# Kernel optimization log

Hardware: AMD Instinct MI355X
Metric: run time of the kernel (lower is better)

## Reference

```python
import jax, jax.numpy as jnp
import numpy as np
from jax import lax

DIM = 1024
INNER = 2048  # dim * expand_factor
STATE = 64
B, T = 4, 2048
DECAY = 0.95
INPUT_FACTOR = 0.05
LN_EPS = 1e-5


def setup_inputs() -> dict:
    key = jax.random.key(0)
    ks = jax.random.split(key, 8)
    s = 0.02  # small weight scale
    return {
        "x": jax.random.normal(ks[0], (B, T, DIM), jnp.float32),
        "W_in": jax.random.normal(ks[1], (2 * INNER, DIM), jnp.float32) * s,
        "conv_w": jax.random.normal(ks[2], (INNER, 1, 4), jnp.float32) * s,
        "conv_b": jax.random.normal(ks[3], (INNER,), jnp.float32) * s,
        "W_B": jax.random.normal(ks[4], (STATE, INNER), jnp.float32) * s,
        "W_C": jax.random.normal(ks[5], (INNER, STATE), jnp.float32) * s,
        "D_param": jax.random.normal(ks[6], (INNER,), jnp.float32) * s,
        "W_out": jax.random.normal(ks[7], (DIM, INNER), jnp.float32) * s,
        "ln_gamma": jnp.ones((DIM,), jnp.float32),
        "ln_beta": jnp.zeros((DIM,), jnp.float32),
    }


def _layernorm(x, g, b):
    mu = jnp.mean(x, axis=-1, keepdims=True)
    var = jnp.mean(jnp.square(x - mu), axis=-1, keepdims=True)
    return (x - mu) * lax.rsqrt(var + LN_EPS) * g + b


def reference(x, W_in, conv_w, conv_b, W_B, W_C, D_param, W_out, ln_gamma, ln_beta):
    Bn, Tn, Dn = x.shape
    # in_proj -> split into input/gate halves
    x_proj = jnp.einsum("btd,ed->bte", x, W_in)  # [B,T,2*INNER]
    x_input, x_gate = jnp.split(x_proj, 2, axis=-1)
    # depthwise causal conv1d (torch pad=3 then slice [:T] == left-pad 3)
    xc = lax.conv_general_dilated(
        x_input.transpose(0, 2, 1),  # [B,C,T]
        conv_w,                       # [C,1,4]
        window_strides=(1,),
        padding=[(3, 0)],
        feature_group_count=INNER,
    ) + conv_b[None, :, None]
    u = jax.nn.silu(xc).transpose(0, 2, 1)  # [B,T,INNER]
    # linear recurrence: h_t = 0.95*h_{t-1} + 0.05*B_proj(u_t); h_0 = 0
    Bu = jnp.einsum("btc,sc->bts", u, W_B)  # [B,T,STATE]

    def step(h, bu_t):
        h = DECAY * h + INPUT_FACTOR * bu_t
        return h, h

    h0 = jnp.zeros((Bn, STATE), x.dtype)
    _, hs = lax.scan(step, h0, Bu.transpose(1, 0, 2))  # hs: [T,B,STATE]
    hs = hs.transpose(1, 0, 2)  # [B,T,STATE]
    y = jnp.einsum("bts,cs->btc", hs, W_C) + D_param * u  # [B,T,INNER]
    y = y * jax.nn.silu(x_gate)
    y = jnp.einsum("btc,dc->btd", y, W_out)  # [B,T,DIM]
    return _layernorm(y + x, ln_gamma, ln_beta)
```

## Files before the change

kernel.cpp:

```cpp
#include <hip/hip_runtime.h>
#include <hip/hip_bf16.h>

#define T_SEQ 2048
#define DIMD  1024
#define INNER 2048
#define STATE 64
#define BATCH 4
#define NCHUNK 64
#define CHUNK_L (T_SEQ / NCHUNK)
#define MROWS (BATCH * T_SEQ)
#define PSTRIDE ((long)MROWS * STATE)

typedef __hip_bfloat16 bf16;
typedef __attribute__((ext_vector_type(8))) short bf16x8v;
typedef __attribute__((ext_vector_type(4))) float f32x4v;
typedef __attribute__((ext_vector_type(4))) short short4v;

__device__ __forceinline__ float b2f(short s) {
    unsigned u = ((unsigned)(unsigned short)s) << 16;
    float f;
    __builtin_memcpy(&f, &u, 4);
    return f;
}
__device__ __forceinline__ short f2b(float f) {
    bf16 h = __float2bfloat16(f);
    short s;
    __builtin_memcpy(&s, &h, 2);
    return s;
}

__device__ __forceinline__ void gld_lds16(void* lds, const void* gsrc) {
    __builtin_amdgcn_global_load_lds(
        (const __attribute__((address_space(1))) unsigned*)gsrc,
        (__attribute__((address_space(3))) unsigned*)lds, 16, 0, 0);
}

template<int N> __device__ __forceinline__ void waitcnt_vm() {
    if constexpr (N == 16)      asm volatile("s_waitcnt vmcnt(16)" ::: "memory");
    else if constexpr (N == 8)  asm volatile("s_waitcnt vmcnt(8)" ::: "memory");
    else if constexpr (N == 6)  asm volatile("s_waitcnt vmcnt(6)" ::: "memory");
    else if constexpr (N == 4)  asm volatile("s_waitcnt vmcnt(4)" ::: "memory");
    else if constexpr (N == 2)  asm volatile("s_waitcnt vmcnt(2)" ::: "memory");
    else                        asm volatile("s_waitcnt vmcnt(0)" ::: "memory");
}
__device__ __forceinline__ void block_barrier() {
    asm volatile("" ::: "memory");
    __builtin_amdgcn_s_barrier();
    asm volatile("" ::: "memory");
}

template<int XSWZ>
__device__ __forceinline__ void swz_block(int& bx, int& by) {
    if constexpr (XSWZ == 1) {
        const int gx = gridDim.x;
        const int nwg = gx * gridDim.y;
        int id = by * gx + bx;
        const int cpx = nwg >> 3;
        id = (id & 7) * cpx + (id >> 3);
        bx = id % gx; by = id / gx;
    } else if constexpr (XSWZ == 2) {
        const int gx = gridDim.x;
        const int gy = gridDim.y;
        const int id = by * gx + bx;
        const int xcd = id & 7;
        const int c   = id >> 3;
        const int rowsX = gy >> 3;
        const int rw  = gx >> 2;
        const int r   = c >> 4;
        const int pos = c & 15;
        const int rbx = (r % rw) << 2;
        const int rby = (r / rw) << 2;
        bx = rbx + (pos & 3);
        by = xcd * rowsX + rby + (pos >> 2);
    }
}

template<int EPI, int XSWZ>
__global__ __launch_bounds__(512, 2)
void gemm_8ph(const short* __restrict__ A, const short* __restrict__ B,
              void* __restrict__ Cout, int M, int N, int K)
{
    __shared__ __align__(16) short As[2][2][128 * 64];
    __shared__ __align__(16) short Bs[2][2][128 * 64];

    int bx = blockIdx.x, by = blockIdx.y;
    swz_block<XSWZ>(bx, by);

    const int tid  = threadIdx.x;
    const int lane = tid & 63;
    const int wave = tid >> 6;
    const int wm2 = (wave >> 2) & 1;
    const int wn2 = wave & 3;
    const long bm = (long)by * 256;
    const long bn = (long)bx * 256;

    const int rsel = lane & 15;
    const int ssrc = (((tid & 7) ^ ((tid >> 3) & 7)) * 8);
    const int swz  = lane & 7;

    f32x4v acc[4][4][2];
#pragma unroll
    for (int q = 0; q < 4; q++)
#pragma unroll
        for (int m = 0; m < 4; m++)
#pragma unroll
            for (int n = 0; n < 2; n++)
                acc[q][m][n] = (f32x4v){0.f, 0.f, 0.f, 0.f};

    const int nt = K / 64;

    auto stage_half = [&](int tt, int h) {
        const int buf = tt & 1;
        const int half = h >> 1;
        const int k0 = tt * 64;
#pragma unroll
        for (int i = 0; i < 2; i++) {
            const int j = i * 512 + tid;
            if (h & 1)
                gld_lds16(&Bs[buf][half][j * 8],
                          &B[(bn + half * 128 + (j >> 3)) * (long)K + k0 + ssrc]);
            else
                gld_lds16(&As[buf][half][j * 8],
                          &A[(bm + half * 128 + (j >> 3)) * (long)K + k0 + ssrc]);
        }
    };

    stage_half(0, 0); stage_half(0, 1); stage_half(0, 2); stage_half(0, 3);

    for (int t = 0; t < nt; ++t) {
        const int buf = t & 1;
        const bool pf = (t + 1 < nt);
#pragma unroll
        for (int h = 0; h < 4; ++h) {
            if (pf) {
                if (h == 0) waitcnt_vm<4>();
                else if (h == 1) waitcnt_vm<4>();
                else if (h == 2) waitcnt_vm<4>();
            } else {
                if (h == 0) waitcnt_vm<4>();
                else if (h == 1) waitcnt_vm<2>();
                else if (h == 2) waitcnt_vm<0>();
            }
            block_barrier();

            const int QM[4] = {0, 1, 1, 0};
            const int QN[4] = {0, 0, 1, 1};
            const int qm = QM[h], qn = QN[h];
            bf16x8v af[4][2], bfv[2][2];
#pragma unroll
            for (int kkh = 0; kkh < 2; kkh++) {
                const int slog = kkh * 4 + (lane >> 4);
                const int soff = ((slog ^ swz) * 8);
#pragma unroll
                for (int m = 0; m < 4; m++) {
                    const int ar = wm2 * 64 + m * 16 + rsel;
                    af[m][kkh] = *(const bf16x8v*)&As[buf][qm][ar * 64 + soff];
                }
#pragma unroll
                for (int n = 0; n < 2; n++) {
                    const int br = wn2 * 32 + n * 16 + rsel;
                    bfv[n][kkh] = *(const bf16x8v*)&Bs[buf][qn][br * 64 + soff];
                }
            }
            if (pf) stage_half(t + 1, h);

            asm volatile("s_waitcnt lgkmcnt(0)" ::: "memory");
            __builtin_amdgcn_sched_barrier(0);
            __builtin_amdgcn_s_setprio(1);
#pragma unroll
            for (int kkh = 0; kkh < 2; kkh++)
#pragma unroll
                for (int m = 0; m < 4; m++)
#pragma unroll
                    for (int n = 0; n < 2; n++)
                        acc[h][m][n] = __builtin_amdgcn_mfma_f32_16x16x32_bf16(
                            af[m][kkh], bfv[n][kkh], acc[h][m][n], 0, 0, 0);
            __builtin_amdgcn_s_setprio(0);
        }
    }

#pragma unroll
    for (int q = 0; q < 4; q++) {
        const int QM[4] = {0, 1, 1, 0};
        const int QN[4] = {0, 0, 1, 1};
#pragma unroll
        for (int m = 0; m < 4; m++) {
#pragma unroll
            for (int n = 0; n < 2; n++) {
                const long col  = bn + QN[q] * 128 + wn2 * 32 + n * 16 + (lane & 15);
                const long row0 = bm + QM[q] * 128 + wm2 * 64 + m * 16 + (lane >> 4) * 4;
#pragma unroll
                for (int j = 0; j < 4; j++) {
                    const long idx = (row0 + j) * (long)N + col;
                    ((short*)Cout)[idx] = f2b(acc[q][m][n][j]);
                }
            }
        }
    }
}

template<int BM, int BN, int BK, int WR, int WC, int EPI, int SPLITK, int XSWZ>
__global__ __launch_bounds__(WR*WC*64, 2)
void gemm_ring(const short* __restrict__ A, const short* __restrict__ B,
               void* __restrict__ Cout, int M, int N, int K,
               const short* __restrict__ u_ptr, const short* __restrict__ gate_ptr,
               const float* __restrict__ Dp)
{
    constexpr int MFR = BM / (WR * 16);
    constexpr int NFR = BN / (WC * 16);
    constexpr int THREADS = WR * WC * 64;
    constexpr int UPR = BK / 8;
    constexpr int AISS = (BM * UPR) / THREADS;
    constexpr int BISS = (BN * UPR) / THREADS;
    constexpr int LPS  = AISS + BISS;
    __shared__ __align__(16) short As[2][BM * BK];
    __shared__ __align__(16) short Bs[2][BN * BK];

    int bx = blockIdx.x, by = blockIdx.y;
    swz_block<XSWZ>(bx, by);

    const int tid  = threadIdx.x;
    const int lane = tid & 63;
    const int wave = tid >> 6;
    const int wm = (wave / WC) * (MFR * 16);
    const int wn = (wave % WC) * (NFR * 16);
    const long bm = (long)by * BM;
    const long bn = (long)bx * BN;

    f32x4v acc[MFR][NFR];
#pragma unroll
    for (int m = 0; m < MFR; m++)
#pragma unroll
        for (int n = 0; n < NFR; n++)
            acc[m][n] = (f32x4v){0.f, 0.f, 0.f, 0.f};

    const int rsel = lane & 15;
    const int ssrc = (((tid & 7) ^ ((tid >> 3) & 7)) * 8);
    const int swz  = lane & 7;

    int kbeg = 0, kend = K;
    if constexpr (SPLITK > 1) {
        const int kch = K / SPLITK;
        kbeg = blockIdx.z * kch;
        kend = kbeg + kch;
    }
    const int nt = (kend - kbeg) / BK;

    auto stage = [&](int buf, int k0) {
#pragma unroll
        for (int i = 0; i < AISS; i++) {
            const int j = i * THREADS + tid;
            gld_lds16(&As[buf][j * 8],
                      &A[(bm + (j >> 3)) * (long)K + k0 + ssrc]);
        }
#pragma unroll
        for (int i = 0; i < BISS; i++) {
            const int j = i * THREADS + tid;
            gld_lds16(&Bs[buf][j * 8],
                      &B[(bn + (j >> 3)) * (long)K + k0 + ssrc]);
        }
    };
    auto compute = [&](int buf) {
#pragma unroll
        for (int kk = 0; kk < BK; kk += 32) {
            const int slog = (kk >> 3) + (lane >> 4);
            const int soff = ((slog ^ swz) * 8);
            bf16x8v af[MFR], bfv[NFR];
#pragma unroll
            for (int m = 0; m < MFR; m++)
                af[m] = *(const bf16x8v*)&As[buf][(wm + m * 16 + rsel) * BK + soff];
#pragma unroll
            for (int n = 0; n < NFR; n++)
                bfv[n] = *(const bf16x8v*)&Bs[buf][(wn + n * 16 + rsel) * BK + soff];
#pragma unroll
            for (int m = 0; m < MFR; m++)
#pragma unroll
                for (int n = 0; n < NFR; n++)
                    acc[m][n] = __builtin_amdgcn_mfma_f32_16x16x32_bf16(
                        af[m], bfv[n], acc[m][n], 0, 0, 0);
        }
    };

    stage(0, kbeg);
    for (int t = 0; t < nt; ++t) {
        const bool pf = (t + 1 < nt);
        if (pf) stage((t + 1) & 1, kbeg + (t + 1) * BK);
        if (pf) waitcnt_vm<LPS>();
        else    waitcnt_vm<0>();
        block_barrier();
        compute(t & 1);
        block_barrier();
    }

    float* fout = (float*)Cout;
    if constexpr (SPLITK > 1)
        fout += (long)blockIdx.z * (long)M * N;

#pragma unroll
    for (int m = 0; m < MFR; m++) {
#pragma unroll
        for (int n = 0; n < NFR; n++) {
            const long col  = bn + wn + n * 16 + (lane & 15);
            const long row0 = bm + wm + m * 16 + (lane >> 4) * 4;
#pragma unroll
            for (int j = 0; j < 4; j++) {
                const long row = row0 + j;
                const float v = acc[m][n][j];
                const long idx = row * (long)N + col;
                if constexpr (EPI == 0) {
                    ((short*)Cout)[idx] = f2b(v);
                } else if constexpr (EPI == 1) {
                    fout[idx] = v;
                } else {
                    ((short*)Cout)[idx] = f2b(v + b2f(u_ptr[idx]));
                }
            }
        }
    }
}

#define EBS 132
__global__ __launch_bounds__(256, 2)
void gemm3_fused(const short* __restrict__ hs, const short* __restrict__ Wc,
                 short* __restrict__ yg, const short* __restrict__ gate_ptr,
                 const float* __restrict__ Dp)
{
    __shared__ __align__(16) short As[128 * 64];
    __shared__ __align__(16) short Bs[128 * 64];
    __shared__ __align__(16) float eb[64 * EBS];

    const int tid  = threadIdx.x;
    const int lane = tid & 63;
    const int wave = tid >> 6;
    const int wm = (wave >> 1) * 64;
    const int wn = (wave & 1) * 64;
    const long bm = (long)blockIdx.y * 128;
    const long bn = (long)blockIdx.x * 128;

    const int rsel = lane & 15;
    const int ssrc = (((tid & 7) ^ ((tid >> 3) & 7)) * 8);
    const int swz  = lane & 7;

#pragma unroll
    for (int i = 0; i < 4; i++) {
        const int j = i * 256 + tid;
        gld_lds16(&As[j * 8], &hs[(bm + (j >> 3)) * (long)STATE + ssrc]);
    }
#pragma unroll
    for (int i = 0; i < 4; i++) {
        const int j = i * 256 + tid;
        gld_lds16(&Bs[j * 8], &Wc[(bn + (j >> 3)) * (long)STATE + ssrc]);
    }
    waitcnt_vm<0>();
    block_barrier();

    f32x4v acc[4][4];
#pragma unroll
    for (int m = 0; m < 4; m++)
#pragma unroll
        for (int n = 0; n < 4; n++)
            acc[m][n] = (f32x4v){0.f, 0.f, 0.f, 0.f};

#pragma unroll
    for (int kk = 0; kk < 64; kk += 32) {
        const int slog = (kk >> 3) + (lane >> 4);
        const int soff = ((slog ^ swz) * 8);
        bf16x8v af[4], bfv[4];
#pragma unroll
        for (int m = 0; m < 4; m++)
            af[m] = *(const bf16x8v*)&As[(wm + m * 16 + rsel) * 64 + soff];
#pragma unroll
        for (int n = 0; n < 4; n++)
            bfv[n] = *(const bf16x8v*)&Bs[(wn + n * 16 + rsel) * 64 + soff];
#pragma unroll
        for (int m = 0; m < 4; m++)
#pragma unroll
            for (int n = 0; n < 4; n++)
                acc[m][n] = __builtin_amdgcn_mfma_f32_16x16x32_bf16(
                    af[m], bfv[n], acc[m][n], 0, 0, 0);
    }

#pragma unroll
    for (int p = 0; p < 2; p++) {
        block_barrier();
        if ((wm >> 6) == p) {
#pragma unroll
            for (int m = 0; m < 4; m++) {
#pragma unroll
                for (int n = 0; n < 4; n++) {
                    const int cl = wn + n * 16 + (lane & 15);
#pragma unroll
                    for (int j = 0; j < 4; j++) {
                        const int rl = m * 16 + (lane >> 4) * 4 + j;
                        eb[rl * EBS + cl] = acc[m][n][j];
                    }
                }
            }
        }
        block_barrier();
#pragma unroll
        for (int k = 0; k < 4; k++) {
            const int unit = k * 256 + tid;
            const int rl = unit >> 4, cg = (unit & 15) * 8;
            const long grow = bm + p * 64 + rl;
            const long gcol = bn + cg;
            f32x4v y0 = *(const f32x4v*)&eb[rl * EBS + cg];
            f32x4v y1 = *(const f32x4v*)&eb[rl * EBS + cg + 4];
            bf16x8v uv = *(const bf16x8v*)&yg[grow * (long)INNER + gcol];
            bf16x8v gv = *(const bf16x8v*)&gate_ptr[grow * (long)(2 * INNER) + gcol];
            short o[8];
#pragma unroll
            for (int i = 0; i < 8; i++) {
                const float yy = (i < 4 ? y0[i] : y1[i - 4]);
                const float uu = b2f(uv[i]);
                const float gg = b2f(gv[i]);
                const float yv = yy + Dp[gcol + i] * uu;
                const float sg = gg / (1.f + __expf(-gg));
                o[i] = f2b(yv * sg);
            }
            *(bf16x8v*)&yg[grow * (long)INNER + gcol] = *(const bf16x8v*)o;
        }
    }
}

__global__ __launch_bounds__(256)
void conv_silu_kernel(const short* __restrict__ xproj, const float* __restrict__ cw,
                      const float* __restrict__ cb, short* __restrict__ u)
{
    const int bt = blockIdx.x;
    const int t  = bt & (T_SEQ - 1);
    const int c0 = threadIdx.x * 8;

    float wreg[4][8];
#pragma unroll
    for (int i = 0; i < 8; i++) {
        float4 wv = *(const float4*)&cw[(c0 + i) * 4];
        wreg[0][i] = wv.x; wreg[1][i] = wv.y; wreg[2][i] = wv.z; wreg[3][i] = wv.w;
    }
    float acc[8];
#pragma unroll
    for (int i = 0; i < 8; i++) acc[i] = cb[c0 + i];

#pragma unroll
    for (int k = 0; k < 4; k++) {
        if (t - 3 + k < 0) continue;
        bf16x8v v = *(const bf16x8v*)&xproj[(long)(bt - 3 + k) * (2 * INNER) + c0];
#pragma unroll
        for (int i = 0; i < 8; i++) acc[i] += b2f(v[i]) * wreg[k][i];
    }
    short o[8];
#pragma unroll
    for (int i = 0; i < 8; i++) {
        float s = acc[i] / (1.f + __expf(-acc[i]));
        o[i] = f2b(s);
    }
    *(bf16x8v*)&u[(long)bt * INNER + c0] = *(const bf16x8v*)o;
}

__global__ __launch_bounds__(64)
void scan_local_kernel(const float* __restrict__ Bu, float* __restrict__ locfin)
{
    const int b  = blockIdx.x / NCHUNK;
    const int ch = blockIdx.x % NCHUNK;
    const long base = ((long)b * T_SEQ + (long)ch * CHUNK_L) * STATE + threadIdx.x;
    float h = 0.f;
#pragma unroll
    for (int t = 0; t < CHUNK_L; t++) {
        const long o = base + (long)t * STATE;
        float bu = (Bu[o] + Bu[o + PSTRIDE]) + (Bu[o + 2 * PSTRIDE] + Bu[o + 3 * PSTRIDE]);
        h = 0.95f * h + 0.05f * bu;
    }
    locfin[(long)blockIdx.x * STATE + threadIdx.x] = h;
}

__global__ __launch_bounds__(256)
void carry_kernel(const float* __restrict__ locfin, float* __restrict__ carry,
                  float decayL)
{
    __shared__ float sm[BATCH * NCHUNK * STATE];
    for (int i = threadIdx.x; i < BATCH * NCHUNK * STATE; i += 256)
        sm[i] = locfin[i];
    __syncthreads();
    const int b = threadIdx.x >> 6, s = threadIdx.x & 63;
    float c = 0.f;
    for (int ch = 0; ch < NCHUNK; ch++) {
        const int idx = (b * NCHUNK + ch) * STATE + s;
        carry[idx] = c;
        c = decayL * c + sm[idx];
    }
}

__global__ __launch_bounds__(64)
void scan_apply_kernel(const float* __restrict__ Bu, const float* __restrict__ carry,
                       short* __restrict__ hs)
{
    const int b  = blockIdx.x / NCHUNK;
    const int ch = blockIdx.x % NCHUNK;
    const long base = ((long)b * T_SEQ + (long)ch * CHUNK_L) * STATE + threadIdx.x;
    float h = carry[(long)blockIdx.x * STATE + threadIdx.x];
#pragma unroll
    for (int t = 0; t < CHUNK_L; t++) {
        const long o = base + (long)t * STATE;
        float bu = (Bu[o] + Bu[o + PSTRIDE]) + (Bu[o + 2 * PSTRIDE] + Bu[o + 3 * PSTRIDE]);
        h = 0.95f * h + 0.05f * bu;
        hs[o] = f2b(h);
    }
}

__global__ __launch_bounds__(256)
void ln_kernel(const short* __restrict__ yx, const float* __restrict__ g,
               const float* __restrict__ b, float* __restrict__ out)
{
    const int row = blockIdx.x;
    const int c   = threadIdx.x * 4;
    const long off = (long)row * DIMD + c;
    const short4v yv = *(const short4v*)&yx[off];
    float s0 = b2f(yv[0]), s1 = b2f(yv[1]), s2 = b2f(yv[2]), s3 = b2f(yv[3]);
    float sum = s0 + s1 + s2 + s3;
    float sq  = s0 * s0 + s1 * s1 + s2 * s2 + s3 * s3;
#pragma unroll
    for (int o = 32; o > 0; o >>= 1) {
        sum += __shfl_down(sum, o);
        sq  += __shfl_down(sq, o);
    }
    __shared__ float rs[4], rq[4];
    const int wave = threadIdx.x >> 6, lane = threadIdx.x & 63;
    if (lane == 0) { rs[wave] = sum; rq[wave] = sq; }
    __syncthreads();
    float tsum = rs[0] + rs[1] + rs[2] + rs[3];
    float tsq  = rq[0] + rq[1] + rq[2] + rq[3];
    float mu  = tsum * (1.f / DIMD);
    float inv = rsqrtf(tsq * (1.f / DIMD) - mu * mu + 1e-5f);
    float4 gv = *(const float4*)&g[c];
    float4 bv = *(const float4*)&b[c];
    float4 ov;
    ov.x = (s0 - mu) * inv * gv.x + bv.x;
    ov.y = (s1 - mu) * inv * gv.y + bv.y;
    ov.z = (s2 - mu) * inv * gv.z + bv.z;
    ov.w = (s3 - mu) * inv * gv.w + bv.w;
    *(float4*)&out[off] = ov;
}

#define C4_X   2097152L
#define C4_W1  (C4_X + 1048576L)
#define C4_WB  (C4_W1 + 32768L)
#define C4_WC  (C4_WB + 32768L)
#define C4_TOT (C4_WC + 524288L)

__global__ __launch_bounds__(256)
void cvt5_kernel(const float* __restrict__ x, const float* __restrict__ w1,
                 const float* __restrict__ wB, const float* __restrict__ wC,
                 const float* __restrict__ wO, short* __restrict__ dst)
{
    const long i = (long)blockIdx.x * 256 + threadIdx.x;
    if (i >= C4_TOT) return;
    const float* s;
    long off;
    if      (i < C4_X)  { s = x;  off = i; }
    else if (i < C4_W1) { s = w1; off = i - C4_X; }
    else if (i < C4_WB) { s = wB; off = i - C4_W1; }
    else if (i < C4_WC) { s = wC; off = i - C4_WB; }
    else                { s = wO; off = i - C4_WC; }
    float4 v = *(const float4*)&s[off * 4];
    short4v o = { f2b(v.x), f2b(v.y), f2b(v.z), f2b(v.w) };
    *(short4v*)&dst[i * 4] = o;
}

extern "C" void kernel_launch(void* const* d_in, const int* in_sizes, int n_in,
                              void* d_out, int out_size, void* d_ws, size_t ws_size,
                              hipStream_t stream)
{
    const float* x     = (const float*)d_in[0];
    const float* W_in  = (const float*)d_in[1];
    const float* cw    = (const float*)d_in[2];
    const float* cb    = (const float*)d_in[3];
    const float* W_B   = (const float*)d_in[4];
    const float* W_C   = (const float*)d_in[5];
    const float* Dp    = (const float*)d_in[6];
    const float* W_out = (const float*)d_in[7];
    const float* ln_g  = (const float*)d_in[8];
    const float* ln_b  = (const float*)d_in[9];

    char* p = (char*)d_ws;
    short* xw    = (short*)(p);
    short* w1    = (short*)(p +  16777216);
    short* wB    = (short*)(p +  25165824);
    short* wC    = (short*)(p +  25427968);
    short* wO    = (short*)(p +  25690112);
    short* xproj = (short*)(p +  29884416);
    short* u     = (short*)(p +  96993280);
    short* hs    = (short*)(p + 132644864);
    short* yg    = u;
    short* yx    = xproj;
    float* BuP    = (float*)(p + 16777216);
    float* locfin = (float*)(p + 25165824);
    float* carry  = (float*)(p + 25231360);

    const int M = MROWS;

    cvt5_kernel<<<(int)((C4_TOT + 255) / 256), 256, 0, stream>>>(
        x, W_in, W_B, W_C, W_out, xw);

    gemm_8ph<0, 2><<<dim3(2 * INNER / 256, M / 256), 512, 0, stream>>>(
        xw, w1, xproj, M, 2 * INNER, DIMD);

    conv_silu_kernel<<<M, 256, 0, stream>>>(xproj, cw, cb, u);

    gemm_ring<64, 64, 64, 2, 2, 1, 4, 0><<<dim3(1, M / 64, 4), 256, 0, stream>>>(
        u, wB, BuP, M, STATE, INNER, nullptr, nullptr, nullptr);

    float decayL;
    {
        double dd = 1.0;
        for (int i = 0; i < CHUNK_L; i++) dd *= 0.95;
        decayL = (float)dd;
    }
    scan_local_kernel<<<BATCH * NCHUNK, STATE, 0, stream>>>(BuP, locfin);
    carry_kernel<<<1, 256, 0, stream>>>(locfin, carry, decayL);
    scan_apply_kernel<<<BATCH * NCHUNK, STATE, 0, stream>>>(BuP, carry, hs);

    gemm3_fused<<<dim3(INNER / 128, M / 128), 256, 0, stream>>>(
        hs, wC, yg, xproj + INNER, Dp);

    gemm_ring<128, 128, 64, 2, 2, 3, 1, 1><<<dim3(DIMD / 128, M / 128), 256, 0, stream>>>(
        yg, wO, yx, M, DIMD, INNER, xw, nullptr, nullptr);

    ln_kernel<<<M, 256, 0, stream>>>(yx, ln_g, ln_b, (float*)d_out);
}
```

Before: 242.8 us.

## Fuse causal conv+SiLU with B-projection GEMM, drop split-K partial sums

```diff
diff --git a/kernel.cpp b/kernel.cpp
--- a/kernel.cpp
+++ b/kernel.cpp
@@ -9,7 +9,6 @@
 #define NCHUNK 64
 #define CHUNK_L (T_SEQ / NCHUNK)
 #define MROWS (BATCH * T_SEQ)
-#define PSTRIDE ((long)MROWS * STATE)
 
 typedef __hip_bfloat16 bf16;
 typedef __attribute__((ext_vector_type(8))) short bf16x8v;
@@ -36,9 +35,7 @@
 }
 
 template<int N> __device__ __forceinline__ void waitcnt_vm() {
-    if constexpr (N == 16)      asm volatile("s_waitcnt vmcnt(16)" ::: "memory");
-    else if constexpr (N == 8)  asm volatile("s_waitcnt vmcnt(8)" ::: "memory");
-    else if constexpr (N == 6)  asm volatile("s_waitcnt vmcnt(6)" ::: "memory");
+    if constexpr (N == 8)       asm volatile("s_waitcnt vmcnt(8)" ::: "memory");
     else if constexpr (N == 4)  asm volatile("s_waitcnt vmcnt(4)" ::: "memory");
     else if constexpr (N == 2)  asm volatile("s_waitcnt vmcnt(2)" ::: "memory");
     else                        asm volatile("s_waitcnt vmcnt(0)" ::: "memory");
@@ -133,9 +130,7 @@
 #pragma unroll
         for (int h = 0; h < 4; ++h) {
             if (pf) {
-                if (h == 0) waitcnt_vm<4>();
-                else if (h == 1) waitcnt_vm<4>();
-                else if (h == 2) waitcnt_vm<4>();
+                if (h < 3) waitcnt_vm<4>();
             } else {
                 if (h == 0) waitcnt_vm<4>();
                 else if (h == 1) waitcnt_vm<2>();
@@ -199,12 +194,11 @@
     }
 }
 
-template<int BM, int BN, int BK, int WR, int WC, int EPI, int SPLITK, int XSWZ>
+template<int BM, int BN, int BK, int WR, int WC, int EPI, int XSWZ>
 __global__ __launch_bounds__(WR*WC*64, 2)
 void gemm_ring(const short* __restrict__ A, const short* __restrict__ B,
                void* __restrict__ Cout, int M, int N, int K,
-               const short* __restrict__ u_ptr, const short* __restrict__ gate_ptr,
-               const float* __restrict__ Dp)
+               const short* __restrict__ u_ptr)
 {
     constexpr int MFR = BM / (WR * 16);
     constexpr int NFR = BN / (WC * 16);
@@ -238,13 +232,7 @@
     const int ssrc = (((tid & 7) ^ ((tid >> 3) & 7)) * 8);
     const int swz  = lane & 7;
 
-    int kbeg = 0, kend = K;
-    if constexpr (SPLITK > 1) {
-        const int kch = K / SPLITK;
-        kbeg = blockIdx.z * kch;
-        kend = kbeg + kch;
-    }
-    const int nt = (kend - kbeg) / BK;
+    const int nt = K / BK;
 
     auto stage = [&](int buf, int k0) {
 #pragma unroll
@@ -281,20 +269,16 @@
         }
     };
 
-    stage(0, kbeg);
+    stage(0, 0);
     for (int t = 0; t < nt; ++t) {
         const bool pf = (t + 1 < nt);
-        if (pf) stage((t + 1) & 1, kbeg + (t + 1) * BK);
+        if (pf) stage((t + 1) & 1, (t + 1) * BK);
         if (pf) waitcnt_vm<LPS>();
         else    waitcnt_vm<0>();
         block_barrier();
         compute(t & 1);
         block_barrier();
     }
-
-    float* fout = (float*)Cout;
-    if constexpr (SPLITK > 1)
-        fout += (long)blockIdx.z * (long)M * N;
 
 #pragma unroll
     for (int m = 0; m < MFR; m++) {
@@ -309,12 +293,103 @@
                 const long idx = row * (long)N + col;
                 if constexpr (EPI == 0) {
                     ((short*)Cout)[idx] = f2b(v);
-                } else if constexpr (EPI == 1) {
-                    fout[idx] = v;
                 } else {
                     ((short*)Cout)[idx] = f2b(v + b2f(u_ptr[idx]));
                 }
             }
+        }
+    }
+}
+
+#define RB 32
+#define CK 256
+__global__ __launch_bounds__(256, 2)
+void conv_bu_kernel(const short* __restrict__ xproj, const float* __restrict__ cw,
+                    const float* __restrict__ cb, const short* __restrict__ wB,
+                    short* __restrict__ u, float* __restrict__ Bu)
+{
+    __shared__ __align__(16) short Us[RB * CK];
+    __shared__ __align__(16) short Ws[STATE * CK];
+
+    const int tid  = threadIdx.x;
+    const int lane = tid & 63;
+    const int wave = tid >> 6;
+    const int wm = (wave >> 1) * 16;
+    const int wn = (wave & 1) * 32;
+    const long r0 = (long)blockIdx.x * RB;
+    const int rsel = lane & 15;
+
+    f32x4v acc[2];
+    acc[0] = (f32x4v){0.f, 0.f, 0.f, 0.f};
+    acc[1] = (f32x4v){0.f, 0.f, 0.f, 0.f};
+
+    for (int ch = 0; ch < INNER / CK; ++ch) {
+        const int k0 = ch * CK;
+#pragma unroll
+        for (int i = 0; i < 8; i++) {
+            const int j = i * 256 + tid;
+            const int row = j >> 5, sp = j & 31;
+            const int sl = sp ^ (row & 7);
+            gld_lds16(&Ws[j * 8], &wB[(long)row * INNER + k0 + sl * 8]);
+        }
+#pragma unroll
+        for (int k = 0; k < 4; k++) {
+            const int unit = k * 256 + tid;
+            const int r = unit >> 5, cg = unit & 31;
+            const long grow = r0 + r;
+            const int t = (int)(grow & (T_SEQ - 1));
+            const int c = k0 + cg * 8;
+            float a[8];
+            {
+                float4 b0 = *(const float4*)&cb[c];
+                float4 b1 = *(const float4*)&cb[c + 4];
+                a[0]=b0.x; a[1]=b0.y; a[2]=b0.z; a[3]=b0.w;
+                a[4]=b1.x; a[5]=b1.y; a[6]=b1.z; a[7]=b1.w;
+            }
+#pragma unroll
+            for (int tap = 0; tap < 4; tap++) {
+                if (t - 3 + tap < 0) continue;
+                bf16x8v v = *(const bf16x8v*)&xproj[(grow - 3 + tap) * (long)(2 * INNER) + c];
+#pragma unroll
+                for (int i = 0; i < 8; i++)
+                    a[i] += b2f(v[i]) * cw[(c + i) * 4 + tap];
+            }
+            short o[8];
+#pragma unroll
+            for (int i = 0; i < 8; i++) {
+                const float s = a[i] / (1.f + __expf(-a[i]));
+                o[i] = f2b(s);
+            }
+            *(bf16x8v*)&u[grow * (long)INNER + c] = *(const bf16x8v*)o;
+            *(bf16x8v*)&Us[r * CK + ((cg ^ (r & 7)) * 8)] = *(const bf16x8v*)o;
+        }
+        waitcnt_vm<0>();
+        block_barrier();
+#pragma unroll
+        for (int kk = 0; kk < CK; kk += 32) {
+            const int slot = (kk >> 3) + (lane >> 4);
+            const int ra = wm + rsel;
+            bf16x8v af = *(const bf16x8v*)&Us[ra * CK + ((slot ^ (ra & 7)) * 8)];
+            bf16x8v bfv[2];
+#pragma unroll
+            for (int n = 0; n < 2; n++) {
+                const int rb = wn + n * 16 + rsel;
+                bfv[n] = *(const bf16x8v*)&Ws[rb * CK + ((slot ^ (rb & 7)) * 8)];
+            }
+#pragma unroll
+            for (int n = 0; n < 2; n++)
+                acc[n] = __builtin_amdgcn_mfma_f32_16x16x32_bf16(af, bfv[n], acc[n], 0, 0, 0);
+        }
+        block_barrier();
+    }
+
+#pragma unroll
+    for (int n = 0; n < 2; n++) {
+        const int col = wn + n * 16 + (lane & 15);
+#pragma unroll
+        for (int j = 0; j < 4; j++) {
+            const int row = wm + (lane >> 4) * 4 + j;
+            Bu[(r0 + row) * (long)STATE + col] = acc[n][j];
         }
     }
 }
@@ -423,40 +498,6 @@
     }
 }
 
-__global__ __launch_bounds__(256)
-void conv_silu_kernel(const short* __restrict__ xproj, const float* __restrict__ cw,
-                      const float* __restrict__ cb, short* __restrict__ u)
-{
-    const int bt = blockIdx.x;
-    const int t  = bt & (T_SEQ - 1);
-    const int c0 = threadIdx.x * 8;
-
-    float wreg[4][8];
-#pragma unroll
-    for (int i = 0; i < 8; i++) {
-        float4 wv = *(const float4*)&cw[(c0 + i) * 4];
-        wreg[0][i] = wv.x; wreg[1][i] = wv.y; wreg[2][i] = wv.z; wreg[3][i] = wv.w;
-    }
-    float acc[8];
-#pragma unroll
-    for (int i = 0; i < 8; i++) acc[i] = cb[c0 + i];
-
-#pragma unroll
-    for (int k = 0; k < 4; k++) {
-        if (t - 3 + k < 0) continue;
-        bf16x8v v = *(const bf16x8v*)&xproj[(long)(bt - 3 + k) * (2 * INNER) + c0];
-#pragma unroll
-        for (int i = 0; i < 8; i++) acc[i] += b2f(v[i]) * wreg[k][i];
-    }
-    short o[8];
-#pragma unroll
-    for (int i = 0; i < 8; i++) {
-        float s = acc[i] / (1.f + __expf(-acc[i]));
-        o[i] = f2b(s);
-    }
-    *(bf16x8v*)&u[(long)bt * INNER + c0] = *(const bf16x8v*)o;
-}
-
 __global__ __launch_bounds__(64)
 void scan_local_kernel(const float* __restrict__ Bu, float* __restrict__ locfin)
 {
@@ -465,11 +506,8 @@
     const long base = ((long)b * T_SEQ + (long)ch * CHUNK_L) * STATE + threadIdx.x;
     float h = 0.f;
 #pragma unroll
-    for (int t = 0; t < CHUNK_L; t++) {
-        const long o = base + (long)t * STATE;
-        float bu = (Bu[o] + Bu[o + PSTRIDE]) + (Bu[o + 2 * PSTRIDE] + Bu[o + 3 * PSTRIDE]);
-        h = 0.95f * h + 0.05f * bu;
-    }
+    for (int t = 0; t < CHUNK_L; t++)
+        h = 0.95f * h + 0.05f * Bu[base + (long)t * STATE];
     locfin[(long)blockIdx.x * STATE + threadIdx.x] = h;
 }
 
@@ -501,8 +539,7 @@
 #pragma unroll
     for (int t = 0; t < CHUNK_L; t++) {
         const long o = base + (long)t * STATE;
-        float bu = (Bu[o] + Bu[o + PSTRIDE]) + (Bu[o + 2 * PSTRIDE] + Bu[o + 3 * PSTRIDE]);
-        h = 0.95f * h + 0.05f * bu;
+        h = 0.95f * h + 0.05f * Bu[o];
         hs[o] = f2b(h);
     }
 }
@@ -592,9 +629,9 @@
     short* hs    = (short*)(p + 132644864);
     short* yg    = u;
     short* yx    = xproj;
-    float* BuP    = (float*)(p + 16777216);
-    float* locfin = (float*)(p + 25165824);
-    float* carry  = (float*)(p + 25231360);
+    float* Bu     = (float*)(p + 16777216);
+    float* locfin = (float*)(p + 18874368);
+    float* carry  = (float*)(p + 18939904);
 
     const int M = MROWS;
 
@@ -604,10 +641,7 @@
     gemm_8ph<0, 2><<<dim3(2 * INNER / 256, M / 256), 512, 0, stream>>>(
         xw, w1, xproj, M, 2 * INNER, DIMD);
 
-    conv_silu_kernel<<<M, 256, 0, stream>>>(xproj, cw, cb, u);
-
-    gemm_ring<64, 64, 64, 2, 2, 1, 4, 0><<<dim3(1, M / 64, 4), 256, 0, stream>>>(
-        u, wB, BuP, M, STATE, INNER, nullptr, nullptr, nullptr);
+    conv_bu_kernel<<<M / RB, 256, 0, stream>>>(xproj, cw, cb, wB, u, Bu);
 
     float decayL;
     {
@@ -615,15 +649,15 @@
         for (int i = 0; i < CHUNK_L; i++) dd *= 0.95;
         decayL = (float)dd;
     }
-    scan_local_kernel<<<BATCH * NCHUNK, STATE, 0, stream>>>(BuP, locfin);
+    scan_local_kernel<<<BATCH * NCHUNK, STATE, 0, stream>>>(Bu, locfin);
     carry_kernel<<<1, 256, 0, stream>>>(locfin, carry, decayL);
-    scan_apply_kernel<<<BATCH * NCHUNK, STATE, 0, stream>>>(BuP, carry, hs);
+    scan_apply_kernel<<<BATCH * NCHUNK, STATE, 0, stream>>>(Bu, carry, hs);
 
     gemm3_fused<<<dim3(INNER / 128, M / 128), 256, 0, stream>>>(
         hs, wC, yg, xproj + INNER, Dp);
 
-    gemm_ring<128, 128, 64, 2, 2, 3, 1, 1><<<dim3(DIMD / 128, M / 128), 256, 0, stream>>>(
-        yg, wO, yx, M, DIMD, INNER, xw, nullptr, nullptr);
+    gemm_ring<128, 128, 64, 2, 2, 3, 1><<<dim3(DIMD / 128, M / 128), 256, 0, stream>>>(
+        yg, wO, yx, M, DIMD, INNER, xw);
 
     ln_kernel<<<M, 256, 0, stream>>>(yx, ln_g, ln_b, (float*)d_out);
 }
```

Result: slower. 282.1 us (+16.2%).
